# Optimization experiments

Measured on AMD Instinct MI355X. Metric: run time of the kernel, lower is better.

## Reference

```python
import jax, jax.numpy as jnp
import numpy as np

B, S, D = 1, 4096, 2048
H = 16
HD = D // H  # 128
BASE = 10000.0


def setup_inputs() -> dict:
    key = jax.random.key(0)
    ks = jax.random.split(key, 6)
    hidden_states = jax.random.normal(ks[0], (B, S, D), dtype=jnp.float32)
    position_ids = jnp.broadcast_to(jnp.arange(S, dtype=jnp.int64 if jax.config.jax_enable_x64 else jnp.int32), (B, S))
    scale = 1.0 / np.sqrt(D)
    Wq = jax.random.normal(ks[1], (D, D), dtype=jnp.float32) * scale
    Wk = jax.random.normal(ks[2], (D, D), dtype=jnp.float32) * scale
    Wv = jax.random.normal(ks[3], (D, D), dtype=jnp.float32) * scale
    Wo = jax.random.normal(ks[4], (D, D), dtype=jnp.float32) * scale
    return {"hidden_states": hidden_states, "Wq": Wq, "Wk": Wk, "Wv": Wv, "Wo": Wo, "position_ids": position_ids}


def _rotate_half(x):
    x1, x2 = x[..., : x.shape[-1] // 2], x[..., x.shape[-1] // 2 :]
    return jnp.concatenate((-x2, x1), axis=-1)


def reference(hidden_states, Wq, Wk, Wv, Wo, position_ids):
    # QKV projections (torch Linear: x @ W.T)
    q = hidden_states @ Wq.T  # [B,S,D]
    k = hidden_states @ Wk.T
    v = hidden_states @ Wv.T
    # split heads -> [B,H,S,HD]
    q = q.reshape(B, S, H, HD).transpose(0, 2, 1, 3)
    k = k.reshape(B, S, H, HD).transpose(0, 2, 1, 3)
    v = v.reshape(B, S, H, HD).transpose(0, 2, 1, 3)
    # RoPE tables over seq positions
    inv_freq = 1.0 / (BASE ** (jnp.arange(0, HD, 2, dtype=jnp.float32) / HD))  # [HD/2]
    t = jnp.arange(S, dtype=jnp.float32)
    freqs = t[:, None] * inv_freq[None, :]            # [S, HD/2]
    emb = jnp.concatenate((freqs, freqs), axis=-1)    # [S, HD]
    cos = jnp.cos(emb)[position_ids][:, None]         # [B,1,S,HD]
    sin = jnp.sin(emb)[position_ids][:, None]
    q = q * cos + _rotate_half(q) * sin
    k = k * cos + _rotate_half(k) * sin
    # attention (num_kv_heads == num_heads, so no GQA repeat)
    scores = jnp.einsum("bhqd,bhkd->bhqk", q, k) / jnp.sqrt(jnp.float32(HD))
    attn = jax.nn.softmax(scores, axis=-1)
    out = jnp.einsum("bhqk,bhkd->bhqd", attn, v)      # [B,H,S,HD]
    out = out.transpose(0, 2, 1, 3).reshape(B, S, D)
    return out @ Wo.T
```

## Files before the change

### kernel.cpp

```cpp
#include <hip/hip_runtime.h>
#include <hip/hip_bf16.h>

#define S_LEN 4096
#define DMODEL 2048
#define NHEADS 16
#define HEADDIM 128
#define LDQ 6144

typedef __attribute__((ext_vector_type(8))) short bf16x8;
typedef __attribute__((ext_vector_type(4))) float f32x4;

__device__ __forceinline__ float bf2f(ushort u) {
  union { unsigned int i; float f; } x; x.i = ((unsigned int)u) << 16; return x.f;
}
__device__ __forceinline__ ushort f2bf(float f) {
  union { float f; unsigned int i; } x; x.f = f;
  unsigned int u = x.i;
  unsigned int r = u + 0x7fffu + ((u >> 16) & 1u);
  return (ushort)(r >> 16);
}
__device__ __forceinline__ unsigned int cvtpk(float a, float b) {
  unsigned int r;
  asm("v_cvt_pk_bf16_f32 %0, %1, %2" : "=v"(r) : "v"(a), "v"(b));
  return r;
}
__device__ __forceinline__ float fexp2(float x) {
  float r;
  asm("v_exp_f32 %0, %1" : "=v"(r) : "v"(x));
  return r;
}

__device__ __forceinline__ void gload16(const ushort* g, ushort* l) {
  __builtin_amdgcn_global_load_lds(
      (const __attribute__((address_space(1))) unsigned int*)g,
      (__attribute__((address_space(3))) unsigned int*)l, 16, 0, 0);
}

__global__ __launch_bounds__(256) void rope_table_kernel(float* __restrict__ cosT,
                                                         float* __restrict__ sinT) {
  int idx = blockIdx.x * 256 + threadIdx.x;
  int t = idx >> 6, j = idx & 63;
  float expo = (float)(2 * j) / 128.0f;
  float inv = 1.0f / powf(10000.0f, expo);
  float f = (float)t * inv;
  cosT[idx] = cosf(f);
  sinT[idx] = sinf(f);
}

__global__ __launch_bounds__(256) void convert_kernel(const float* __restrict__ in,
                                                      ushort* __restrict__ hi) {
  int i = (blockIdx.x * 256 + threadIdx.x) * 4;
  float4 v = *reinterpret_cast<const float4*>(&in[i]);
  ushort4 h;
  h.x = f2bf(v.x); h.y = f2bf(v.y); h.z = f2bf(v.z); h.w = f2bf(v.w);
  *reinterpret_cast<ushort4*>(&hi[i]) = h;
}

__global__ __launch_bounds__(256) void prep_weights(const float* __restrict__ Wq,
                                                    const float* __restrict__ Wk,
                                                    const float* __restrict__ Wv,
                                                    const float* __restrict__ Wo,
                                                    ushort* __restrict__ Wqkv,
                                                    ushort* __restrict__ Woh) {
  int i = (blockIdx.x * 256 + threadIdx.x) * 4;
  int which = blockIdx.y;
  const float* src = (which == 0) ? Wq : (which == 1) ? Wk : (which == 2) ? Wv : Wo;
  ushort* dst = (which == 3) ? Woh : (Wqkv + (size_t)which * DMODEL * DMODEL);
  float4 v = *reinterpret_cast<const float4*>(&src[i]);
  ushort4 h;
  h.x = f2bf(v.x); h.y = f2bf(v.y); h.z = f2bf(v.z); h.w = f2bf(v.w);
  *reinterpret_cast<ushort4*>(&dst[i]) = h;
}

__global__ __launch_bounds__(256) void gemm_qkv(const ushort* __restrict__ Ah_,
                                                const ushort* __restrict__ Bh_,
                                                ushort* __restrict__ Cout,
                                                int M, int N, int K) {
  __shared__ __align__(16) ushort sAh[128 * 64], sBh[128 * 64];
  const int tid = threadIdx.x;
  const int wave = tid >> 6, lane = tid & 63;
  const int lg = lane >> 4, lm = lane & 15;
  const int nwg = gridDim.x * gridDim.y;
  const int id = blockIdx.y * gridDim.x + blockIdx.x;
  const int cpx = nwg >> 3;
  const int swz = (id & 7) * cpx + (id >> 3);
  const int nbx = N >> 7;
  const int m0 = (swz / nbx) * 128, n0 = (swz % nbx) * 128;
  const int wm = (wave >> 1) * 64, wn = (wave & 1) * 64;
  f32x4 acc[4][4] = {};

  int srow[4], scc[4], lbs[4];
#pragma unroll
  for (int it = 0; it < 4; ++it) {
    int ci = it * 256 + wave * 64 + lane;
    srow[it] = ci >> 3;
    scc[it] = (ci & 7) ^ (srow[it] & 7);
    lbs[it] = (it * 256 + wave * 64) * 8;
  }

  for (int k0 = 0; k0 < K; k0 += 64) {
    __syncthreads();
#pragma unroll
    for (int it = 0; it < 4; ++it) {
      size_t ga = (size_t)(m0 + srow[it]) * K + k0 + scc[it] * 8;
      size_t gb = (size_t)(n0 + srow[it]) * K + k0 + scc[it] * 8;
      gload16(&Ah_[ga], &sAh[lbs[it]]);
      gload16(&Bh_[gb], &sBh[lbs[it]]);
    }
    __syncthreads();
    bf16x8 ah[4][2], bh[4][2];
#pragma unroll
    for (int t = 0; t < 4; ++t)
#pragma unroll
      for (int kc = 0; kc < 2; ++kc) {
        int Ra = wm + t * 16 + lm;
        int Rb = wn + t * 16 + lm;
        int pa_ = ((kc * 4 + lg) ^ (Ra & 7)) * 8;
        int pb_ = ((kc * 4 + lg) ^ (Rb & 7)) * 8;
        ah[t][kc] = *reinterpret_cast<const bf16x8*>(&sAh[Ra * 64 + pa_]);
        bh[t][kc] = *reinterpret_cast<const bf16x8*>(&sBh[Rb * 64 + pb_]);
      }
#pragma unroll
    for (int kc = 0; kc < 2; ++kc)
#pragma unroll
      for (int mi = 0; mi < 4; ++mi)
#pragma unroll
        for (int ni = 0; ni < 4; ++ni)
          acc[mi][ni] = __builtin_amdgcn_mfma_f32_16x16x32_bf16(ah[mi][kc], bh[ni][kc], acc[mi][ni], 0, 0, 0);
  }
#pragma unroll
  for (int mi = 0; mi < 4; ++mi)
#pragma unroll
    for (int ni = 0; ni < 4; ++ni)
#pragma unroll
      for (int j = 0; j < 4; ++j) {
        int row = m0 + wm + mi * 16 + lg * 4 + j;
        int col = n0 + wn + ni * 16 + lm;
        Cout[(size_t)row * N + col] = f2bf(acc[mi][ni][j]);
      }
}

__global__ __launch_bounds__(256) void gemm1o(const ushort* __restrict__ Ah_,
                                              const ushort* __restrict__ Bh_,
                                              float* __restrict__ Cout,
                                              int M, int N, int K) {
  __shared__ __align__(16) ushort sAh[128 * 32], sBh[128 * 32];
  const int tid = threadIdx.x;
  const int wave = tid >> 6, lane = tid & 63;
  const int lg = lane >> 4, lm = lane & 15;
  const int nwg = gridDim.x * gridDim.y;
  const int id = blockIdx.y * gridDim.x + blockIdx.x;
  const int cpx = nwg >> 3;
  const int swz = (id & 7) * cpx + (id >> 3);
  const int nbx = N >> 7;
  const int m0 = (swz / nbx) * 128, n0 = (swz % nbx) * 128;
  const int wm = (wave >> 1) * 64, wn = (wave & 1) * 64;
  f32x4 acc[4][4] = {};

  for (int k0 = 0; k0 < K; k0 += 32) {
    __syncthreads();
#pragma unroll
    for (int t = 0; t < 2; ++t) {
      int r = wave * 32 + t * 16 + (lane >> 2);
      int ca = (lane & 3) ^ ((r >> 1) & 3);
      size_t ga = (size_t)(m0 + r) * K + k0 + ca * 8;
      size_t gb = (size_t)(n0 + r) * K + k0 + ca * 8;
      int lb = (wave * 32 + t * 16) * 32;
      gload16(&Ah_[ga], &sAh[lb]);
      gload16(&Bh_[gb], &sBh[lb]);
    }
    __syncthreads();
    bf16x8 ah[4], bh[4];
#pragma unroll
    for (int t = 0; t < 4; ++t) {
      int Ra = wm + t * 16 + lm;
      int Rb = wn + t * 16 + lm;
      int ca = (lg ^ ((Ra >> 1) & 3)) * 8;
      int cb = (lg ^ ((Rb >> 1) & 3)) * 8;
      ah[t] = *reinterpret_cast<const bf16x8*>(&sAh[Ra * 32 + ca]);
      bh[t] = *reinterpret_cast<const bf16x8*>(&sBh[Rb * 32 + cb]);
    }
#pragma unroll
    for (int mi = 0; mi < 4; ++mi)
#pragma unroll
      for (int ni = 0; ni < 4; ++ni)
        acc[mi][ni] = __builtin_amdgcn_mfma_f32_16x16x32_bf16(ah[mi], bh[ni], acc[mi][ni], 0, 0, 0);
  }
#pragma unroll
  for (int mi = 0; mi < 4; ++mi)
#pragma unroll
    for (int ni = 0; ni < 4; ++ni)
#pragma unroll
      for (int j = 0; j < 4; ++j) {
        int row = m0 + wm + mi * 16 + lg * 4 + j;
        int col = n0 + wn + ni * 16 + lm;
        Cout[(size_t)row * N + col] = acc[mi][ni][j];
      }
}

__global__ __launch_bounds__(256) void rope2_kernel(ushort* __restrict__ QKV,
                                                    const int* __restrict__ pos,
                                                    const float* __restrict__ cosT,
                                                    const float* __restrict__ sinT) {
  int t = blockIdx.x * 256 + threadIdx.x;
  int j0 = (t & 7) * 8;
  int hh = (t >> 3) & 15;
  int s = t >> 7;
  int p = pos[s];
  float cs[8], sn[8];
  *reinterpret_cast<float4*>(&cs[0]) = *reinterpret_cast<const float4*>(&cosT[p * 64 + j0]);
  *reinterpret_cast<float4*>(&cs[4]) = *reinterpret_cast<const float4*>(&cosT[p * 64 + j0 + 4]);
  *reinterpret_cast<float4*>(&sn[0]) = *reinterpret_cast<const float4*>(&sinT[p * 64 + j0]);
  *reinterpret_cast<float4*>(&sn[4]) = *reinterpret_cast<const float4*>(&sinT[p * 64 + j0 + 4]);
  size_t base = (size_t)s * LDQ + hh * HEADDIM + j0;
  union u8 { uint4 v; ushort e[8]; };
  u8 qa, qb, ka, kb;
  qa.v = *reinterpret_cast<const uint4*>(&QKV[base]);
  qb.v = *reinterpret_cast<const uint4*>(&QKV[base + 64]);
  ka.v = *reinterpret_cast<const uint4*>(&QKV[base + DMODEL]);
  kb.v = *reinterpret_cast<const uint4*>(&QKV[base + DMODEL + 64]);
  const float scl = 0.12751742f;
#pragma unroll
  for (int e = 0; e < 8; ++e) {
    float q1 = bf2f(qa.e[e]), q2 = bf2f(qb.e[e]);
    float k1 = bf2f(ka.e[e]), k2 = bf2f(kb.e[e]);
    qa.e[e] = f2bf((q1 * cs[e] - q2 * sn[e]) * scl);
    qb.e[e] = f2bf((q2 * cs[e] + q1 * sn[e]) * scl);
    ka.e[e] = f2bf(k1 * cs[e] - k2 * sn[e]);
    kb.e[e] = f2bf(k2 * cs[e] + k1 * sn[e]);
  }
  *reinterpret_cast<uint4*>(&QKV[base]) = qa.v;
  *reinterpret_cast<uint4*>(&QKV[base + 64]) = qb.v;
  *reinterpret_cast<uint4*>(&QKV[base + DMODEL]) = ka.v;
  *reinterpret_cast<uint4*>(&QKV[base + DMODEL + 64]) = kb.v;
}

__global__ __launch_bounds__(256) void transpose_kernel(const ushort* __restrict__ Vr,
                                                        ushort* __restrict__ Vt) {
  __shared__ __align__(16) ushort tile[64 * 72];
  int tid = threadIdx.x;
  int s0 = blockIdx.x * 64, c0 = blockIdx.y * 64;
#pragma unroll
  for (int it = 0; it < 2; ++it) {
    int i = tid + it * 256;
    int r = i >> 3, c = i & 7;
    *reinterpret_cast<uint4*>(&tile[r * 72 + c * 8]) =
        *reinterpret_cast<const uint4*>(&Vr[(size_t)(s0 + r) * LDQ + c0 + c * 8]);
  }
  __syncthreads();
#pragma unroll
  for (int it = 0; it < 2; ++it) {
    int i = tid + it * 256;
    int cr = i >> 3, sc = i & 7;
    ushort tmp[8];
#pragma unroll
    for (int j = 0; j < 8; ++j) tmp[j] = tile[(sc * 8 + j) * 72 + cr];
    *reinterpret_cast<uint4*>(&Vt[(size_t)(c0 + cr) * S_LEN + s0 + sc * 8]) =
        *reinterpret_cast<uint4*>(tmp);
  }
}

__global__ __launch_bounds__(256, 2) void flash12_kernel(const ushort* __restrict__ QKV,
                                                         const ushort* __restrict__ Vt,
                                                         ushort* __restrict__ Oh) {
  __shared__ __align__(16) ushort Kt[2][64 * 128];
  __shared__ __align__(16) ushort Vs[2][128 * 64];
  const int tid = threadIdx.x;
  const int wave = tid >> 6, lane = tid & 63;
  const int lg = lane >> 4, lm = lane & 15;
  const int id = blockIdx.y * gridDim.x + blockIdx.x;
  const int o = (id & 7) * 64 + (id >> 3);
  const int h = o >> 5;
  const int q0 = (o & 31) * 128;

  bf16x8 qh[2][4];
#pragma unroll
  for (int t2 = 0; t2 < 2; ++t2) {
    int qrow = q0 + wave * 32 + t2 * 16 + lm;
#pragma unroll
    for (int kc = 0; kc < 4; ++kc)
      qh[t2][kc] = *reinterpret_cast<const bf16x8*>(
          &QKV[(size_t)qrow * LDQ + h * HEADDIM + kc * 32 + lg * 8]);
  }

  bf16x8 ones;
#pragma unroll
  for (int i = 0; i < 8; ++i) ones[i] = (short)0x3f80;

  auto rho = [](int s) {
    return 32 * ((s >> 4) & 1) + 8 * ((s >> 2) & 3) + 4 * (s >> 5) + (s & 3);
  };
  const ushort* Kb = QKV + DMODEL;
  const ushort* pK[4];
  const ushort* pV[4];
  int lbs[4];
#pragma unroll
  for (int k = 0; k < 4; ++k) {
    int ci = k * 256 + wave * 64 + lane;
    int ks = ci >> 4;
    int kcc = (ci & 15) ^ (ks & 7);
    pK[k] = Kb + (size_t)rho(ks) * LDQ + h * HEADDIM + kcc * 8;
    int vd = ci >> 3;
    int vcc = (ci & 7) ^ (vd & 7);
    pV[k] = Vt + (size_t)(h * HEADDIM + vd) * S_LEN + vcc * 8;
    lbs[k] = (k * 256 + wave * 64) * 8;
  }

  f32x4 oacc[2][8] = {};
  f32x4 osum[2] = {};
  float mrun[2];
#pragma unroll
  for (int t2 = 0; t2 < 2; ++t2) mrun[t2] = -3.0e38f;

#pragma unroll
  for (int k = 0; k < 4; ++k) {
    gload16(pK[k], &Kt[0][lbs[k]]);
    gload16(pV[k], &Vs[0][lbs[k]]);
  }
  __syncthreads();

  for (int t = 0; t < S_LEN / 64; ++t) {
    const int cur = t & 1;
    if (t < S_LEN / 64 - 1) {
      const size_t koff = (size_t)(t + 1) * 64;
#pragma unroll
      for (int k = 0; k < 4; ++k) {
        gload16(pK[k] + koff * LDQ, &Kt[cur ^ 1][lbs[k]]);
        gload16(pV[k] + koff, &Vs[cur ^ 1][lbs[k]]);
      }
    }
    const ushort* Kc = &Kt[cur][0];
    const ushort* Vc = &Vs[cur][0];

    f32x4 st[2][4] = {};
    __builtin_amdgcn_s_setprio(1);
#pragma unroll
    for (int nf = 0; nf < 4; ++nf)
#pragma unroll
      for (int kc = 0; kc < 4; ++kc) {
        int pc = (kc * 4 + lg) ^ (lm & 7);
        bf16x8 kfrag = *reinterpret_cast<const bf16x8*>(&Kc[(nf * 16 + lm) * 128 + pc * 8]);
        st[0][nf] = __builtin_amdgcn_mfma_f32_16x16x32_bf16(kfrag, qh[0][kc], st[0][nf], 0, 0, 0);
        st[1][nf] = __builtin_amdgcn_mfma_f32_16x16x32_bf16(kfrag, qh[1][kc], st[1][nf], 0, 0, 0);
      }
    __builtin_amdgcn_s_setprio(0);

    float m16[2];
#pragma unroll
    for (int t2 = 0; t2 < 2; ++t2) {
      float m = fmaxf(st[t2][0][0], st[t2][0][1]);
      m = fmaxf(fmaxf(m, st[t2][0][2]), st[t2][0][3]);
      m = fmaxf(fmaxf(m, st[t2][1][0]), st[t2][1][1]);
      m = fmaxf(fmaxf(m, st[t2][1][2]), st[t2][1][3]);
      m = fmaxf(fmaxf(m, st[t2][2][0]), st[t2][2][1]);
      m = fmaxf(fmaxf(m, st[t2][2][2]), st[t2][2][3]);
      m = fmaxf(fmaxf(m, st[t2][3][0]), st[t2][3][1]);
      m = fmaxf(fmaxf(m, st[t2][3][2]), st[t2][3][3]);
      m = fmaxf(m, __shfl_xor(m, 16));
      m = fmaxf(m, __shfl_xor(m, 32));
      m16[t2] = m;
    }

    bool grow = (m16[0] > mrun[0] + 11.5f) || (m16[1] > mrun[1] + 11.5f);
    if (__any(grow)) {
#pragma unroll
      for (int t2 = 0; t2 < 2; ++t2) {
        float mn = fmaxf(mrun[t2], m16[t2]);
        float scl = fexp2(mrun[t2] - mn);
        mrun[t2] = mn;
        float sj[4];
#pragma unroll
        for (int j = 0; j < 4; ++j) sj[j] = __shfl(scl, lg * 4 + j);
#pragma unroll
        for (int j = 0; j < 4; ++j) osum[t2][j] *= sj[j];
#pragma unroll
        for (int nb = 0; nb < 8; ++nb)
#pragma unroll
          for (int j = 0; j < 4; ++j) oacc[t2][nb][j] *= sj[j];
      }
    }

#pragma unroll
    for (int t2 = 0; t2 < 2; ++t2)
#pragma unroll
      for (int nf = 0; nf < 4; ++nf)
#pragma unroll
        for (int j = 0; j < 4; ++j)
          st[t2][nf][j] = fexp2(st[t2][nf][j] - mrun[t2]);

    bf16x8 pa[2][2];
#pragma unroll
    for (int t2 = 0; t2 < 2; ++t2)
#pragma unroll
      for (int kk = 0; kk < 2; ++kk) {
        union { unsigned int u[4]; bf16x8 v; } w_;
        w_.u[0] = cvtpk(st[t2][kk][0], st[t2][kk][1]);
        w_.u[1] = cvtpk(st[t2][kk][2], st[t2][kk][3]);
        w_.u[2] = cvtpk(st[t2][2 + kk][0], st[t2][2 + kk][1]);
        w_.u[3] = cvtpk(st[t2][2 + kk][2], st[t2][2 + kk][3]);
        pa[t2][kk] = w_.v;
      }

    __builtin_amdgcn_s_setprio(1);
#pragma unroll
    for (int t2 = 0; t2 < 2; ++t2) {
      osum[t2] = __builtin_amdgcn_mfma_f32_16x16x32_bf16(pa[t2][0], ones, osum[t2], 0, 0, 0);
      osum[t2] = __builtin_amdgcn_mfma_f32_16x16x32_bf16(pa[t2][1], ones, osum[t2], 0, 0, 0);
    }
#pragma unroll
    for (int nb = 0; nb < 8; ++nb)
#pragma unroll
      for (int kk = 0; kk < 2; ++kk) {
        int pc = (kk * 4 + lg) ^ (lm & 7);
        bf16x8 vfrag = *reinterpret_cast<const bf16x8*>(&Vc[(nb * 16 + lm) * 64 + pc * 8]);
        oacc[0][nb] = __builtin_amdgcn_mfma_f32_16x16x32_bf16(pa[0][kk], vfrag, oacc[0][nb], 0, 0, 0);
        oacc[1][nb] = __builtin_amdgcn_mfma_f32_16x16x32_bf16(pa[1][kk], vfrag, oacc[1][nb], 0, 0, 0);
      }
    __builtin_amdgcn_s_setprio(0);

    __syncthreads();
  }

#pragma unroll
  for (int t2 = 0; t2 < 2; ++t2) {
    float linv[4];
#pragma unroll
    for (int j = 0; j < 4; ++j) linv[j] = 1.0f / osum[t2][j];
#pragma unroll
    for (int nb = 0; nb < 8; ++nb)
#pragma unroll
      for (int j = 0; j < 4; ++j) {
        int row = q0 + wave * 32 + t2 * 16 + lg * 4 + j;
        int col = h * HEADDIM + nb * 16 + lm;
        Oh[(size_t)row * DMODEL + col] = f2bf(oacc[t2][nb][j] * linv[j]);
      }
  }
}

extern "C" void kernel_launch(void* const* d_in, const int* in_sizes, int n_in,
                              void* d_out, int out_size, void* d_ws, size_t ws_size,
                              hipStream_t stream) {
  (void)in_sizes; (void)n_in; (void)out_size; (void)ws_size;
  const float* X  = (const float*)d_in[0];
  const float* Wq = (const float*)d_in[1];
  const float* Wk = (const float*)d_in[2];
  const float* Wv = (const float*)d_in[3];
  const float* Wo = (const float*)d_in[4];
  const int* pos  = (const int*)d_in[5];
  float* out = (float*)d_out;

  ushort* wb = (ushort*)d_ws;
  const size_t SD = (size_t)S_LEN * DMODEL;
  const size_t DD = (size_t)DMODEL * DMODEL;

  ushort* Xh   = wb;
  ushort* QKV  = wb + 2 * SD;
  ushort* Vt   = wb + 5 * SD;
  ushort* W0h  = wb + 6 * SD;
  ushort* Wqkv = wb + 7 * SD;
  float* cosT  = (float*)(wb + 9 * SD);
  float* sinT  = cosT + (size_t)S_LEN * 64;
  ushort* OhB  = Wqkv;

  rope_table_kernel<<<S_LEN * 64 / 256, 256, 0, stream>>>(cosT, sinT);
  convert_kernel<<<SD / 1024, 256, 0, stream>>>(X, Xh);
  prep_weights<<<dim3(DD / 1024, 4), 256, 0, stream>>>(Wq, Wk, Wv, Wo, Wqkv, W0h);

  gemm_qkv<<<dim3(LDQ / 128, S_LEN / 128), 256, 0, stream>>>(Xh, Wqkv, QKV, S_LEN, LDQ, DMODEL);

  rope2_kernel<<<(S_LEN * 1024 / 8) / 256, 256, 0, stream>>>(QKV, pos, cosT, sinT);
  transpose_kernel<<<dim3(S_LEN / 64, DMODEL / 64), 256, 0, stream>>>(QKV + 2 * DMODEL, Vt);

  flash12_kernel<<<dim3(32, 16), 256, 0, stream>>>(QKV, Vt, OhB);

  dim3 gemmGrid(DMODEL / 128, S_LEN / 128);
  gemm1o<<<gemmGrid, 256, 0, stream>>>(OhB, W0h, out, S_LEN, DMODEL, DMODEL);
}
```

Measured before the change: 349.9 us.

## Split attention over two KV halves with combine kernel

```diff
diff --git a/kernel.cpp b/kernel.cpp
--- a/kernel.cpp
+++ b/kernel.cpp
@@ -260,18 +260,22 @@
   }
 }
 
-__global__ __launch_bounds__(256, 2) void flash12_kernel(const ushort* __restrict__ QKV,
+__global__ __launch_bounds__(256, 4) void flash13_kernel(const ushort* __restrict__ QKV,
                                                          const ushort* __restrict__ Vt,
-                                                         ushort* __restrict__ Oh) {
-  __shared__ __align__(16) ushort Kt[2][64 * 128];
-  __shared__ __align__(16) ushort Vs[2][128 * 64];
+                                                         ushort* __restrict__ Op,
+                                                         float* __restrict__ Mv,
+                                                         float* __restrict__ Lv) {
+  __shared__ __align__(16) ushort Kt[2][32 * 128];
+  __shared__ __align__(16) ushort Vs[2][64 * 64];
   const int tid = threadIdx.x;
   const int wave = tid >> 6, lane = tid & 63;
   const int lg = lane >> 4, lm = lane & 15;
   const int id = blockIdx.y * gridDim.x + blockIdx.x;
+  const int z = blockIdx.z;
   const int o = (id & 7) * 64 + (id >> 3);
   const int h = o >> 5;
   const int q0 = (o & 31) * 128;
+  const size_t kbase = (size_t)z * 2048;
 
   bf16x8 qh[2][4];
 #pragma unroll
@@ -287,22 +291,21 @@
 #pragma unroll
   for (int i = 0; i < 8; ++i) ones[i] = (short)0x3f80;
 
-  auto rho = [](int s) {
-    return 32 * ((s >> 4) & 1) + 8 * ((s >> 2) & 3) + 4 * (s >> 5) + (s & 3);
-  };
   const ushort* Kb = QKV + DMODEL;
-  const ushort* pK[4];
-  const ushort* pV[4];
-  int lbs[4];
-#pragma unroll
-  for (int k = 0; k < 4; ++k) {
+  const ushort* pK[2];
+  const ushort* pV[2];
+  int lbs[2];
+#pragma unroll
+  for (int k = 0; k < 2; ++k) {
     int ci = k * 256 + wave * 64 + lane;
     int ks = ci >> 4;
     int kcc = (ci & 15) ^ (ks & 7);
-    pK[k] = Kb + (size_t)rho(ks) * LDQ + h * HEADDIM + kcc * 8;
-    int vd = ci >> 3;
-    int vcc = (ci & 7) ^ (vd & 7);
-    pV[k] = Vt + (size_t)(h * HEADDIM + vd) * S_LEN + vcc * 8;
+    int krho = 8 * ((ks >> 2) & 3) + 4 * ((ks >> 4) & 1) + (ks & 3);
+    pK[k] = Kb + (kbase + krho) * LDQ + h * HEADDIM + kcc * 8;
+    int vr = ci >> 3;
+    int vc = (ci & 7) ^ (vr & 7);
+    int vd = 2 * vr + (vc >> 2);
+    pV[k] = Vt + (size_t)(h * HEADDIM + vd) * S_LEN + kbase + (vc & 3) * 8;
     lbs[k] = (k * 256 + wave * 64) * 8;
   }
 
@@ -313,29 +316,28 @@
   for (int t2 = 0; t2 < 2; ++t2) mrun[t2] = -3.0e38f;
 
 #pragma unroll
-  for (int k = 0; k < 4; ++k) {
+  for (int k = 0; k < 2; ++k) {
     gload16(pK[k], &Kt[0][lbs[k]]);
     gload16(pV[k], &Vs[0][lbs[k]]);
   }
   __syncthreads();
 
-  for (int t = 0; t < S_LEN / 64; ++t) {
+  for (int t = 0; t < 64; ++t) {
     const int cur = t & 1;
-    if (t < S_LEN / 64 - 1) {
-      const size_t koff = (size_t)(t + 1) * 64;
-#pragma unroll
-      for (int k = 0; k < 4; ++k) {
-        gload16(pK[k] + koff * LDQ, &Kt[cur ^ 1][lbs[k]]);
-        gload16(pV[k] + koff, &Vs[cur ^ 1][lbs[k]]);
+    if (t < 63) {
+#pragma unroll
+      for (int k = 0; k < 2; ++k) {
+        gload16(pK[k] + (size_t)(t + 1) * 32 * LDQ, &Kt[cur ^ 1][lbs[k]]);
+        gload16(pV[k] + (size_t)(t + 1) * 32, &Vs[cur ^ 1][lbs[k]]);
       }
     }
     const ushort* Kc = &Kt[cur][0];
     const ushort* Vc = &Vs[cur][0];
 
-    f32x4 st[2][4] = {};
+    f32x4 st[2][2] = {};
     __builtin_amdgcn_s_setprio(1);
 #pragma unroll
-    for (int nf = 0; nf < 4; ++nf)
+    for (int nf = 0; nf < 2; ++nf)
 #pragma unroll
       for (int kc = 0; kc < 4; ++kc) {
         int pc = (kc * 4 + lg) ^ (lm & 7);
@@ -352,10 +354,6 @@
       m = fmaxf(fmaxf(m, st[t2][0][2]), st[t2][0][3]);
       m = fmaxf(fmaxf(m, st[t2][1][0]), st[t2][1][1]);
       m = fmaxf(fmaxf(m, st[t2][1][2]), st[t2][1][3]);
-      m = fmaxf(fmaxf(m, st[t2][2][0]), st[t2][2][1]);
-      m = fmaxf(fmaxf(m, st[t2][2][2]), st[t2][2][3]);
-      m = fmaxf(fmaxf(m, st[t2][3][0]), st[t2][3][1]);
-      m = fmaxf(fmaxf(m, st[t2][3][2]), st[t2][3][3]);
       m = fmaxf(m, __shfl_xor(m, 16));
       m = fmaxf(m, __shfl_xor(m, 32));
       m16[t2] = m;
@@ -383,58 +381,88 @@
 #pragma unroll
     for (int t2 = 0; t2 < 2; ++t2)
 #pragma unroll
-      for (int nf = 0; nf < 4; ++nf)
+      for (int nf = 0; nf < 2; ++nf)
 #pragma unroll
         for (int j = 0; j < 4; ++j)
           st[t2][nf][j] = fexp2(st[t2][nf][j] - mrun[t2]);
 
-    bf16x8 pa[2][2];
-#pragma unroll
-    for (int t2 = 0; t2 < 2; ++t2)
-#pragma unroll
-      for (int kk = 0; kk < 2; ++kk) {
-        union { unsigned int u[4]; bf16x8 v; } w_;
-        w_.u[0] = cvtpk(st[t2][kk][0], st[t2][kk][1]);
-        w_.u[1] = cvtpk(st[t2][kk][2], st[t2][kk][3]);
-        w_.u[2] = cvtpk(st[t2][2 + kk][0], st[t2][2 + kk][1]);
-        w_.u[3] = cvtpk(st[t2][2 + kk][2], st[t2][2 + kk][3]);
-        pa[t2][kk] = w_.v;
-      }
+    bf16x8 pa[2];
+#pragma unroll
+    for (int t2 = 0; t2 < 2; ++t2) {
+      union { unsigned int u[4]; bf16x8 v; } w_;
+      w_.u[0] = cvtpk(st[t2][0][0], st[t2][0][1]);
+      w_.u[1] = cvtpk(st[t2][0][2], st[t2][0][3]);
+      w_.u[2] = cvtpk(st[t2][1][0], st[t2][1][1]);
+      w_.u[3] = cvtpk(st[t2][1][2], st[t2][1][3]);
+      pa[t2] = w_.v;
+    }
 
     __builtin_amdgcn_s_setprio(1);
-#pragma unroll
-    for (int t2 = 0; t2 < 2; ++t2) {
-      osum[t2] = __builtin_amdgcn_mfma_f32_16x16x32_bf16(pa[t2][0], ones, osum[t2], 0, 0, 0);
-      osum[t2] = __builtin_amdgcn_mfma_f32_16x16x32_bf16(pa[t2][1], ones, osum[t2], 0, 0, 0);
-    }
-#pragma unroll
-    for (int nb = 0; nb < 8; ++nb)
-#pragma unroll
-      for (int kk = 0; kk < 2; ++kk) {
-        int pc = (kk * 4 + lg) ^ (lm & 7);
-        bf16x8 vfrag = *reinterpret_cast<const bf16x8*>(&Vc[(nb * 16 + lm) * 64 + pc * 8]);
-        oacc[0][nb] = __builtin_amdgcn_mfma_f32_16x16x32_bf16(pa[0][kk], vfrag, oacc[0][nb], 0, 0, 0);
-        oacc[1][nb] = __builtin_amdgcn_mfma_f32_16x16x32_bf16(pa[1][kk], vfrag, oacc[1][nb], 0, 0, 0);
-      }
+    osum[0] = __builtin_amdgcn_mfma_f32_16x16x32_bf16(pa[0], ones, osum[0], 0, 0, 0);
+    osum[1] = __builtin_amdgcn_mfma_f32_16x16x32_bf16(pa[1], ones, osum[1], 0, 0, 0);
+#pragma unroll
+    for (int nb = 0; nb < 8; ++nb) {
+      int vr = nb * 8 + (lm >> 1);
+      int pc = ((lm & 1) * 4 + lg) ^ (vr & 7);
+      bf16x8 vfrag = *reinterpret_cast<const bf16x8*>(&Vc[vr * 64 + pc * 8]);
+      oacc[0][nb] = __builtin_amdgcn_mfma_f32_16x16x32_bf16(pa[0], vfrag, oacc[0][nb], 0, 0, 0);
+      oacc[1][nb] = __builtin_amdgcn_mfma_f32_16x16x32_bf16(pa[1], vfrag, oacc[1][nb], 0, 0, 0);
+    }
     __builtin_amdgcn_s_setprio(0);
 
     __syncthreads();
   }
 
+  Op += (size_t)z * S_LEN * DMODEL;
 #pragma unroll
   for (int t2 = 0; t2 < 2; ++t2) {
-    float linv[4];
-#pragma unroll
-    for (int j = 0; j < 4; ++j) linv[j] = 1.0f / osum[t2][j];
 #pragma unroll
     for (int nb = 0; nb < 8; ++nb)
 #pragma unroll
       for (int j = 0; j < 4; ++j) {
         int row = q0 + wave * 32 + t2 * 16 + lg * 4 + j;
         int col = h * HEADDIM + nb * 16 + lm;
-        Oh[(size_t)row * DMODEL + col] = f2bf(oacc[t2][nb][j] * linv[j]);
-      }
-  }
+        Op[(size_t)row * DMODEL + col] = f2bf(oacc[t2][nb][j]);
+      }
+    if (lm == 0) {
+#pragma unroll
+      for (int j = 0; j < 4; ++j) {
+        int row = q0 + wave * 32 + t2 * 16 + lg * 4 + j;
+        Lv[(size_t)z * 65536 + row * 16 + h] = osum[t2][j];
+      }
+    }
+    if (lg == 0) {
+      int row = q0 + wave * 32 + t2 * 16 + lm;
+      Mv[(size_t)z * 65536 + row * 16 + h] = mrun[t2];
+    }
+  }
+}
+
+__global__ __launch_bounds__(256) void combine_kernel(const ushort* __restrict__ Op0,
+                                                      const ushort* __restrict__ Op1,
+                                                      const float* __restrict__ Mv,
+                                                      const float* __restrict__ Lv,
+                                                      ushort* __restrict__ Oh) {
+  int idx = blockIdx.x * 256 + threadIdx.x;
+  int q = idx >> 8;
+  int col = (idx & 255) * 8;
+  int h = col >> 7;
+  int mi = q * 16 + h;
+  float m0 = Mv[mi], m1 = Mv[65536 + mi];
+  float l0 = Lv[mi], l1 = Lv[65536 + mi];
+  float m = fmaxf(m0, m1);
+  float w0 = fexp2(m0 - m), w1 = fexp2(m1 - m);
+  float inv = 1.0f / (l0 * w0 + l1 * w1);
+  w0 *= inv; w1 *= inv;
+  union u8 { uint4 v; ushort e[8]; };
+  u8 a, b, o;
+  size_t off = (size_t)q * DMODEL + col;
+  a.v = *reinterpret_cast<const uint4*>(&Op0[off]);
+  b.v = *reinterpret_cast<const uint4*>(&Op1[off]);
+#pragma unroll
+  for (int e = 0; e < 8; ++e)
+    o.e[e] = f2bf(bf2f(a.e[e]) * w0 + bf2f(b.e[e]) * w1);
+  *reinterpret_cast<uint4*>(&Oh[off]) = o.v;
 }
 
 extern "C" void kernel_launch(void* const* d_in, const int* in_sizes, int n_in,
@@ -454,12 +482,16 @@
   const size_t DD = (size_t)DMODEL * DMODEL;
 
   ushort* Xh   = wb;
+  ushort* Op0  = wb;
+  ushort* Op1  = wb + SD;
   ushort* QKV  = wb + 2 * SD;
   ushort* Vt   = wb + 5 * SD;
   ushort* W0h  = wb + 6 * SD;
   ushort* Wqkv = wb + 7 * SD;
   float* cosT  = (float*)(wb + 9 * SD);
   float* sinT  = cosT + (size_t)S_LEN * 64;
+  float* Mv    = cosT;
+  float* Lv    = cosT + 2 * 65536;
   ushort* OhB  = Wqkv;
 
   rope_table_kernel<<<S_LEN * 64 / 256, 256, 0, stream>>>(cosT, sinT);
@@ -471,7 +503,8 @@
   rope2_kernel<<<(S_LEN * 1024 / 8) / 256, 256, 0, stream>>>(QKV, pos, cosT, sinT);
   transpose_kernel<<<dim3(S_LEN / 64, DMODEL / 64), 256, 0, stream>>>(QKV + 2 * DMODEL, Vt);
 
-  flash12_kernel<<<dim3(32, 16), 256, 0, stream>>>(QKV, Vt, OhB);
+  flash13_kernel<<<dim3(32, 16, 2), 256, 0, stream>>>(QKV, Vt, Op0, Mv, Lv);
+  combine_kernel<<<(S_LEN * DMODEL / 8) / 256, 256, 0, stream>>>(Op0, Op1, Mv, Lv, OhB);
 
   dim3 gemmGrid(DMODEL / 128, S_LEN / 128);
   gemm1o<<<gemmGrid, 256, 0, stream>>>(OhB, W0h, out, S_LEN, DMODEL, DMODEL);
```

New measurement: 498.9 us. 42.6% more time.
